# Performance work log

Measured on AMD Instinct MI355X. Metric: run time of the kernel, lower is better.

The kernel has to match this reference:

```python
import jax, jax.numpy as jnp
import numpy as np

# AdaptiveLogSoftmaxWithLoss config (input_dim=2048, n_classes=50257, div_value=4.0)
CUTOFFS = [1000, 10000, 50257]  # torch appends n_classes
N_CLUSTERS = 2                   # len(CUTOFFS) - 1
HEAD_SIZE = CUTOFFS[0] + N_CLUSTERS  # 1002
D = 2048
HSZ = [D // 4, D // 16]          # tail hidden sizes: [512, 128]
N_TOK = 4096


def setup_inputs() -> dict:
    key = jax.random.key(0)
    ks = jax.random.split(key, 7)
    w = 0.02  # weight scale so logits stay O(1)
    x = jax.random.normal(ks[0], (N_TOK, D), dtype=jnp.float32)
    W_head = jax.random.normal(ks[1], (HEAD_SIZE, D), dtype=jnp.float32) * w
    W1_0 = jax.random.normal(ks[2], (HSZ[0], D), dtype=jnp.float32) * w
    W2_0 = jax.random.normal(ks[3], (CUTOFFS[1] - CUTOFFS[0], HSZ[0]), dtype=jnp.float32) * w  # [9000, 512]
    W1_1 = jax.random.normal(ks[4], (HSZ[1], D), dtype=jnp.float32) * w
    W2_1 = jax.random.normal(ks[5], (CUTOFFS[2] - CUTOFFS[1], HSZ[1]), dtype=jnp.float32) * w  # [40257, 128]
    target = jax.random.randint(ks[6], (N_TOK,), 0, CUTOFFS[2], dtype=jnp.int32)
    return {"x": x, "target": target, "W_head": W_head,
            "W1_0": W1_0, "W2_0": W2_0, "W1_1": W1_1, "W2_1": W2_1}


def reference(x, target, W_head, W1_0, W2_0, W1_1, W2_1):
    # head: [N, 1002] = [1000 frequent classes | 2 cluster logits]
    head = x @ W_head.T
    head_lsm = jax.nn.log_softmax(head, axis=-1)

    t = target
    # log-prob of target if it lies in the head (clip keeps gather in-range; masked later)
    head_lp = jnp.take_along_axis(head_lsm, jnp.clip(t, 0, CUTOFFS[0] - 1)[:, None], axis=1)[:, 0]

    def tail_target_lp(W1, W2, low, high, cluster_idx):
        # two-stage projection: [N,D] @ [D,h] @ [h,osz]
        logits = (x @ W1.T) @ W2.T                     # [N, high-low]
        lsm = jax.nn.log_softmax(logits, axis=-1)
        idx = jnp.clip(t - low, 0, high - low - 1)
        g = jnp.take_along_axis(lsm, idx[:, None], axis=1)[:, 0]
        # combine with head's cluster log-prob
        return head_lsm[:, CUTOFFS[0] + cluster_idx] + g

    lp0 = tail_target_lp(W1_0, W2_0, CUTOFFS[0], CUTOFFS[1], 0)
    lp1 = tail_target_lp(W1_1, W2_1, CUTOFFS[1], CUTOFFS[2], 1)

    out = jnp.where(t < CUTOFFS[0], head_lp, jnp.where(t < CUTOFFS[1], lp0, lp1))
    loss = -jnp.mean(out)
    return out, loss
```

## Files before the change

kernel.cpp:

```cpp
#include <hip/hip_runtime.h>
#include <hip/hip_bf16.h>
#include <math.h>

#define NTOK 4096
#define DIM 2048
#define NHEAD 1002
#define NCAT 1664
#define C0LO 1000
#define C0HI 10000
#define OSZ0 9000
#define OSZ1 40257
#define H0S 512
#define H1S 128
#define JS0 32
#define JS1 16
#define HEADBLKS 8
#define NT0 141
#define NT1 315
#define PROJB 416
#define CVTB 352

typedef __attribute__((ext_vector_type(4))) short short4v;
typedef __attribute__((ext_vector_type(8))) short short8v;
typedef __attribute__((ext_vector_type(4))) float f32x4;
typedef __hip_bfloat16 bf16;

#define GLOBAL_AS __attribute__((address_space(1)))
#define LDS_AS __attribute__((address_space(3)))

#define RAW_BAR() __builtin_amdgcn_s_barrier()
#define SCHED_FENCE() __builtin_amdgcn_sched_barrier(0)
#define WAIT_VM(N) asm volatile("s_waitcnt vmcnt(" #N ")" ::: "memory")
#define WAIT_LGKM0() asm volatile("s_waitcnt lgkmcnt(0)" ::: "memory")

__device__ __forceinline__ int kperm(int c) {
  return (c & ~31) | (((c & 15) >> 2) << 3) | (((c >> 4) & 1) << 2) | (c & 3);
}

__device__ __forceinline__ void cvt8(const float* s1, const float* s2, bf16* dst) {
  union { short8v v; bf16 h[8]; } u;
  float4 a = *reinterpret_cast<const float4*>(s1);
  float4 b = *reinterpret_cast<const float4*>(s2);
  u.h[0] = __float2bfloat16(a.x); u.h[1] = __float2bfloat16(a.y);
  u.h[2] = __float2bfloat16(a.z); u.h[3] = __float2bfloat16(a.w);
  u.h[4] = __float2bfloat16(b.x); u.h[5] = __float2bfloat16(b.y);
  u.h[6] = __float2bfloat16(b.z); u.h[7] = __float2bfloat16(b.w);
  *reinterpret_cast<short8v*>(dst) = u.v;
}

__global__ __launch_bounds__(256) void cvt_xw(
    const float* __restrict__ x, const float* __restrict__ W_head,
    const float* __restrict__ W1_0, const float* __restrict__ W1_1,
    bf16* __restrict__ xb, bf16* __restrict__ Wcat) {
  const long NX = (long)NTOK * DIM / 8;
  const long NC = (long)NCAT * DIM / 8;
  long gid = (long)blockIdx.x * 256 + threadIdx.x;
  if (gid < NX) {
    long rel = gid * 8;
    long c1 = (rel & ~31L) + ((rel >> 3) & 3) * 4;
    cvt8(x + c1, x + c1 + 16, xb + rel);
  } else if (gid < NX + NC) {
    long rel = (gid - NX) * 8;
    int row = (int)(rel >> 11);
    long c1 = (rel & ~31L) + ((rel >> 3) & 3) * 4;
    int col = (int)(c1 & 2047);
    const float* srow = nullptr;
    if (row < NHEAD) srow = W_head + (long)row * DIM;
    else if (row < 1024) srow = nullptr;
    else if (row < 1536) srow = W1_0 + (long)(row - 1024) * DIM;
    else srow = W1_1 + (long)(row - 1536) * DIM;
    if (srow) {
      cvt8(srow + col, srow + col + 16, Wcat + rel);
    } else {
      union { short8v v; bf16 h[8]; } u;
#pragma unroll
      for (int e = 0; e < 8; ++e) u.h[e] = __float2bfloat16(0.f);
      *reinterpret_cast<short8v*>(Wcat + rel) = u.v;
    }
  }
}

__device__ __forceinline__ void stage_tile(const bf16* __restrict__ g, int row0,
                                           int maxrow, int ld, int k0,
                                           char* lds, int wave, int lane) {
#pragma unroll
  for (int c = 0; c < 4; ++c) {
    int rbase = wave * 32 + c * 8;
    int row = rbase + (lane >> 3);
    int grow = row0 + row;
    grow = grow < maxrow ? grow : maxrow;
    int slot = (lane & 7) ^ (row & 7);
    const bf16* src = g + (size_t)grow * ld + k0 + slot * 8;
    __builtin_amdgcn_global_load_lds((const GLOBAL_AS unsigned int*)src,
                                     (LDS_AS unsigned int*)(lds + rbase * 128),
                                     16, 0, 0);
  }
}

__device__ __forceinline__ void stage_tileB64(const bf16* __restrict__ g, int row0,
                                              int maxrow, int ld, int k0,
                                              char* lds, int wave, int lane) {
#pragma unroll
  for (int c = 0; c < 2; ++c) {
    int rbase = wave * 16 + c * 8;
    int row = rbase + (lane >> 3);
    int grow = row0 + row;
    grow = grow < maxrow ? grow : maxrow;
    int slot = (lane & 7) ^ (row & 7);
    const bf16* src = g + (size_t)grow * ld + k0 + slot * 8;
    __builtin_amdgcn_global_load_lds((const GLOBAL_AS unsigned int*)src,
                                     (LDS_AS unsigned int*)(lds + rbase * 128),
                                     16, 0, 0);
  }
}

__device__ __forceinline__ void stage_tile256(const bf16* __restrict__ g, int row0,
                                              int maxrow, int ld,
                                              char* lds, int wave, int lane) {
#pragma unroll
  for (int c = 0; c < 8; ++c) {
    int rbase = wave * 32 + c * 4;
    int row = rbase + (lane >> 4);
    int grow = row0 + row;
    grow = grow < maxrow ? grow : maxrow;
    int slot = (lane & 15) ^ (row & 7);
    const bf16* src = g + (size_t)grow * ld + slot * 8;
    __builtin_amdgcn_global_load_lds((const GLOBAL_AS unsigned int*)src,
                                     (LDS_AS unsigned int*)(lds + rbase * 256),
                                     16, 0, 0);
  }
}

__device__ __forceinline__ short8v read_frag(const char* lds, int row, int kk, int lane) {
  int slot = (kk * 4 + (lane >> 4)) ^ (row & 7);
  return *reinterpret_cast<const short8v*>(lds + row * 128 + slot * 16);
}
__device__ __forceinline__ short8v read_frag256(const char* lds, int row, int kk, int lane) {
  int slot = (kk * 4 + (lane >> 4)) ^ (row & 7);
  return *reinterpret_cast<const short8v*>(lds + row * 256 + slot * 16);
}

__device__ __forceinline__ void reduce_write_ps(float srun[4][4], float* reds,
                                                float* ps, int slice, int tok0,
                                                int lane, int wr, int wc) {
#pragma unroll
  for (int off = 1; off < 16; off <<= 1)
#pragma unroll
    for (int m = 0; m < 4; ++m)
#pragma unroll
      for (int r = 0; r < 4; ++r) srun[m][r] += __shfl_xor(srun[m][r], off);
  __syncthreads();
  if (wc == 0 && (lane & 15) == 0) {
#pragma unroll
    for (int m = 0; m < 4; ++m)
#pragma unroll
      for (int r = 0; r < 4; ++r)
        reds[wr * 64 + m * 16 + (lane >> 4) * 4 + r] = srun[m][r];
  }
  __syncthreads();
  if (wc == 1 && (lane & 15) == 0) {
#pragma unroll
    for (int m = 0; m < 4; ++m)
#pragma unroll
      for (int r = 0; r < 4; ++r) {
        int row = wr * 64 + m * 16 + (lane >> 4) * 4 + r;
        ps[(size_t)slice * NTOK + tok0 + row] = reds[row] + srun[m][r];
      }
  }
}

__global__ __launch_bounds__(256, 4) void tail0_lse(
    const bf16* __restrict__ Ab, const bf16* __restrict__ W2b,
    float* __restrict__ ps) {
  __shared__ __align__(16) char As[16384];
  __shared__ __align__(16) char Bs[8192];
  __shared__ float reds[128];
  int tid = threadIdx.x;
  int lane = tid & 63, wave = tid >> 6;
  int wr = wave >> 1, wc = wave & 1;
  int tok0 = blockIdx.x * 128;
  int ys = blockIdx.y;
  int t_lo = (NT0 * ys) / JS0, t_hi = (NT0 * (ys + 1)) / JS0;
  float srun[4][4] = {};
  for (int jt = t_lo; jt < t_hi; ++jt) {
    int j0 = jt * 64;
    f32x4 acc[4][2] = {};
    for (int k0 = 0; k0 < H0S; k0 += 64) {
      __syncthreads();
      stage_tile(Ab, tok0, NTOK - 1, H0S, k0, As, wave, lane);
      stage_tileB64(W2b, j0, OSZ0 - 1, H0S, k0, Bs, wave, lane);
      __syncthreads();
#pragma unroll
      for (int kk = 0; kk < 2; ++kk) {
        short8v af[4], bfr[2];
#pragma unroll
        for (int m = 0; m < 4; ++m)
          af[m] = read_frag(As, wr * 64 + m * 16 + (lane & 15), kk, lane);
#pragma unroll
        for (int n = 0; n < 2; ++n)
          bfr[n] = read_frag(Bs, wc * 32 + n * 16 + (lane & 15), kk, lane);
#pragma unroll
        for (int m = 0; m < 4; ++m)
#pragma unroll
          for (int n = 0; n < 2; ++n)
            acc[m][n] = __builtin_amdgcn_mfma_f32_16x16x32_bf16(af[m], bfr[n], acc[m][n], 0, 0, 0);
      }
    }
#pragma unroll
    for (int m = 0; m < 4; ++m)
#pragma unroll
      for (int n = 0; n < 2; ++n) {
        int col = j0 + wc * 32 + n * 16 + (lane & 15);
        if (col < OSZ0) {
#pragma unroll
          for (int r = 0; r < 4; ++r) srun[m][r] += __expf(acc[m][n][r]);
        }
      }
  }
  reduce_write_ps(srun, reds, ps, ys, tok0, lane, wr, wc);
}

__device__ void tail1_body(const bf16* __restrict__ Ab, const bf16* __restrict__ W2b,
                           float* __restrict__ ps, char* lds) {
  char* buf0 = lds;
  char* buf1 = lds + 32768;
  float* reds = (float*)(lds + 65536);
  int tid = threadIdx.x;
  int lane = tid & 63, wave = tid >> 6;
  int wr = wave >> 1, wc = wave & 1;
  int tok0 = blockIdx.x * 128;
  int ys = blockIdx.y;
  int t_lo = (NT1 * ys) / JS1, t_hi = (NT1 * (ys + 1)) / JS1;
  int nt = t_hi - t_lo;

  stage_tile256(Ab, tok0, NTOK - 1, H1S, buf1, wave, lane);
  WAIT_VM(0); SCHED_FENCE();
  RAW_BAR();
  short8v afr[4][4];
#pragma unroll
  for (int kk = 0; kk < 4; ++kk)
#pragma unroll
    for (int m = 0; m < 4; ++m)
      afr[kk][m] = read_frag256(buf1, wr * 64 + m * 16 + (lane & 15), kk, lane);
  stage_tile256(W2b, t_lo * 128, OSZ1 - 1, H1S, buf0, wave, lane);
  WAIT_LGKM0(); SCHED_FENCE();
  RAW_BAR();
  if (nt > 1) stage_tile256(W2b, (t_lo + 1) * 128, OSZ1 - 1, H1S, buf1, wave, lane);

  float srun[4][4] = {};
  for (int i = 0; i < nt; ++i) {
    char* cur = (i & 1) ? buf1 : buf0;
    if (i + 1 < nt) { WAIT_VM(8); } else { WAIT_VM(0); }
    SCHED_FENCE();
    RAW_BAR();
    int j0 = (t_lo + i) * 128;
    f32x4 acc[4][4] = {};
#pragma unroll
    for (int kk = 0; kk < 4; ++kk) {
      short8v bfr[4];
#pragma unroll
      for (int n = 0; n < 4; ++n)
        bfr[n] = read_frag256(cur, wc * 64 + n * 16 + (lane & 15), kk, lane);
#pragma unroll
      for (int m = 0; m < 4; ++m)
#pragma unroll
        for (int n = 0; n < 4; ++n)
          acc[m][n] = __builtin_amdgcn_mfma_f32_16x16x32_bf16(afr[kk][m], bfr[n], acc[m][n], 0, 0, 0);
    }
#pragma unroll
    for (int m = 0; m < 4; ++m)
#pragma unroll
      for (int n = 0; n < 4; ++n) {
        int col = j0 + wc * 64 + n * 16 + (lane & 15);
        if (col < OSZ1) {
#pragma unroll
          for (int r = 0; r < 4; ++r) srun[m][r] += __expf(acc[m][n][r]);
        }
      }
    SCHED_FENCE();
    RAW_BAR();
    if (i + 2 < nt) stage_tile256(W2b, (t_lo + i + 2) * 128, OSZ1 - 1, H1S, cur, wave, lane);
  }
  reduce_write_ps(srun, reds, ps, ys, tok0, lane, wr, wc);
}

__global__ __launch_bounds__(256, 2) void tail1_lse(
    const bf16* __restrict__ Ab, const bf16* __restrict__ W2b,
    float* __restrict__ ps) {
  __shared__ __align__(16) char lds[66048];
  tail1_body(Ab, W2b, ps, lds);
}

__global__ __launch_bounds__(256, 3) void proj_plus(
    const bf16* __restrict__ A, const bf16* __restrict__ B,
    const float* __restrict__ W2_0, const float* __restrict__ W2_1,
    bf16* __restrict__ W20b, bf16* __restrict__ W21b,
    float* __restrict__ head, float* __restrict__ h0, bf16* __restrict__ h0b,
    float* __restrict__ h1, bf16* __restrict__ h1b, float* __restrict__ ps_head) {
  __shared__ __align__(16) char As[16384];
  __shared__ __align__(16) char Bs[16384];
  __shared__ float reds[128];
  if (blockIdx.x >= PROJB) {
    const long N20 = (long)OSZ0 * H0S / 8;
    const long N21 = (long)OSZ1 * H1S / 8;
    long idx = (long)(blockIdx.x - PROJB) * 256 + threadIdx.x;
    const long stride = (long)CVTB * 256;
    for (; idx < N20 + N21; idx += stride) {
      long rel; const float* srcb; bf16* dstb;
      if (idx < N20) { rel = idx * 8;          srcb = W2_0; dstb = W20b; }
      else           { rel = (idx - N20) * 8;  srcb = W2_1; dstb = W21b; }
      long c1 = (rel & ~31L) + ((rel >> 3) & 3) * 4;
      cvt8(srcb + c1, srcb + c1 + 16, dstb + rel);
    }
    return;
  }
  int tid = threadIdx.x;
  int lane = tid & 63, wave = tid >> 6;
  int wr = wave >> 1, wc = wave & 1;
  int wgid = blockIdx.x;
  int cx = wgid & 7, w = wgid >> 3;
  int col_b = w >> 2;
  int row_b = cx * 4 + (w & 3);
  int row0 = row_b * 128, col0 = col_b * 128;
  f32x4 acc[4][4] = {};
  for (int k0 = 0; k0 < DIM; k0 += 64) {
    __syncthreads();
    stage_tile(A, row0, NTOK - 1, DIM, k0, As, wave, lane);
    stage_tile(B, col0, NCAT - 1, DIM, k0, Bs, wave, lane);
    __syncthreads();
#pragma unroll
    for (int kk = 0; kk < 2; ++kk) {
      short8v af[4], bfr[4];
#pragma unroll
      for (int m = 0; m < 4; ++m)
        af[m] = read_frag(As, wr * 64 + m * 16 + (lane & 15), kk, lane);
#pragma unroll
      for (int n = 0; n < 4; ++n)
        bfr[n] = read_frag(Bs, wc * 64 + n * 16 + (lane & 15), kk, lane);
#pragma unroll
      for (int m = 0; m < 4; ++m)
#pragma unroll
        for (int n = 0; n < 4; ++n)
          acc[m][n] = __builtin_amdgcn_mfma_f32_16x16x32_bf16(af[m], bfr[n], acc[m][n], 0, 0, 0);
    }
  }
  float srun[4][4] = {};
#pragma unroll
  for (int m = 0; m < 4; ++m) {
    int row = row0 + wr * 64 + m * 16 + (lane >> 4) * 4;
#pragma unroll
    for (int n = 0; n < 4; ++n) {
      int col = col0 + wc * 64 + n * 16 + (lane & 15);
#pragma unroll
      for (int r = 0; r < 4; ++r) {
        float v = acc[m][n][r];
        if (col < NHEAD) {
          head[(size_t)(row + r) * NHEAD + col] = v;
          srun[m][r] += __expf(v);
        } else if (col >= 1024 && col < 1536) {
          int c = col - 1024;
          h0[(size_t)(row + r) * H0S + c] = v;
          h0b[(size_t)(row + r) * H0S + kperm(c)] = __float2bfloat16(v);
        } else if (col >= 1536) {
          int c = col - 1536;
          h1[(size_t)(row + r) * H1S + c] = v;
          h1b[(size_t)(row + r) * H1S + kperm(c)] = __float2bfloat16(v);
        }
      }
    }
  }
  if (col_b < HEADBLKS) {
    reduce_write_ps(srun, reds, ps_head, col_b, row0, lane, wr, wc);
  }
}

__global__ __launch_bounds__(256) void finalize2(
    const int* __restrict__ target, const float* __restrict__ head,
    const float* __restrict__ ps_head,
    const float* __restrict__ h0, const float* __restrict__ h1,
    const float* __restrict__ W2_0, const float* __restrict__ W2_1,
    const float* __restrict__ ps0, const float* __restrict__ ps1,
    float* __restrict__ out) {
  int warp = threadIdx.x >> 6, lane = threadIdx.x & 63;
  int i = blockIdx.x * 4 + warp;
  if (i >= NTOK) return;
  int t = target[i];
  float sh = 0.f;
#pragma unroll
  for (int s = 0; s < HEADBLKS; ++s) sh += ps_head[(size_t)s * NTOK + i];
  float lse_head = logf(sh);
  float res;
  if (t < C0LO) {
    res = head[(size_t)i * NHEAD + t] - lse_head;
  } else {
    int c = (t < C0HI) ? 0 : 1;
    int H = c ? H1S : H0S;
    int low = c ? C0HI : C0LO;
    const float* hv = (c ? h1 : h0) + (size_t)i * H;
    const float* wv = (c ? W2_1 : W2_0) + (size_t)(t - low) * H;
    float p = 0.f;
    for (int k = lane * 4; k < H; k += 256) {
      float4 a = *reinterpret_cast<const float4*>(hv + k);
      float4 b = *reinterpret_cast<const float4*>(wv + k);
      p += a.x * b.x + a.y * b.y + a.z * b.z + a.w * b.w;
    }
#pragma unroll
    for (int off = 32; off > 0; off >>= 1) p += __shfl_xor(p, off);
    const float* ps = c ? ps1 : ps0;
    int js = c ? JS1 : JS0;
    float S = 0.f;
    for (int s = 0; s < js; ++s) S += ps[(size_t)s * NTOK + i];
    float cl = head[(size_t)i * NHEAD + C0LO + c];
    res = (cl - lse_head) + (p - logf(S));
  }
  if (lane == 0) out[i] = res;
}

__global__ __launch_bounds__(256) void loss_kernel(float* __restrict__ out) {
  __shared__ float red[256];
  int tid = threadIdx.x;
  float s = 0.f;
  for (int j = tid; j < NTOK; j += 256) s += out[j];
  red[tid] = s; __syncthreads();
  for (int off = 128; off > 0; off >>= 1) {
    if (tid < off) red[tid] += red[tid + off];
    __syncthreads();
  }
  if (tid == 0) out[NTOK] = -red[0] / (float)NTOK;
}

extern "C" void kernel_launch(void* const* d_in, const int* in_sizes, int n_in,
                              void* d_out, int out_size, void* d_ws, size_t ws_size,
                              hipStream_t stream) {
  (void)in_sizes; (void)n_in; (void)out_size; (void)ws_size;
  const float* x = (const float*)d_in[0];
  const int* target = (const int*)d_in[1];
  const float* W_head = (const float*)d_in[2];
  const float* W1_0 = (const float*)d_in[3];
  const float* W2_0 = (const float*)d_in[4];
  const float* W1_1 = (const float*)d_in[5];
  const float* W2_1 = (const float*)d_in[6];
  float* out = (float*)d_out;

  char* w = (char*)d_ws;
  size_t off = 0;
  auto alloc = [&](size_t bytes) -> void* {
    void* p = w + off;
    off = (off + bytes + 255) & ~(size_t)255;
    return p;
  };
  bf16* xb   = (bf16*)alloc((size_t)NTOK * DIM * 2);
  bf16* Wcat = (bf16*)alloc((size_t)NCAT * DIM * 2);
  bf16* W20b = (bf16*)alloc((size_t)OSZ0 * H0S * 2);
  bf16* W21b = (bf16*)alloc((size_t)OSZ1 * H1S * 2);
  float* head = (float*)alloc((size_t)NTOK * NHEAD * 4);
  float* h0   = (float*)alloc((size_t)NTOK * H0S * 4);
  bf16*  h0b  = (bf16*)alloc((size_t)NTOK * H0S * 2);
  float* h1   = (float*)alloc((size_t)NTOK * H1S * 4);
  bf16*  h1b  = (bf16*)alloc((size_t)NTOK * H1S * 2);
  float* ps_head = (float*)alloc((size_t)HEADBLKS * NTOK * 4);
  float* ps0 = (float*)alloc((size_t)JS0 * NTOK * 4);
  float* ps1 = (float*)alloc((size_t)JS1 * NTOK * 4);

  dim3 blk(256);
  const long NXW = (long)NTOK * DIM / 8 + (long)NCAT * DIM / 8;
  cvt_xw<<<dim3((unsigned)((NXW + 255) / 256)), blk, 0, stream>>>(
      x, W_head, W1_0, W1_1, xb, Wcat);

  proj_plus<<<dim3(PROJB + CVTB), blk, 0, stream>>>(
      xb, Wcat, W2_0, W2_1, W20b, W21b, head, h0, h0b, h1, h1b, ps_head);

  tail0_lse<<<dim3(NTOK / 128, JS0), blk, 0, stream>>>(h0b, W20b, ps0);
  tail1_lse<<<dim3(NTOK / 128, JS1), blk, 0, stream>>>(h1b, W21b, ps1);

  finalize2<<<dim3(NTOK / 4), blk, 0, stream>>>(target, head, ps_head, h0, h1,
                                                W2_0, W2_1, ps0, ps1, out);
  loss_kernel<<<1, blk, 0, stream>>>(out);
}
```

Before: 174.9 us.

## Widen tail1 blocks to 8 waves covering 256 tokens per W2 tile

```diff
diff --git a/kernel.cpp b/kernel.cpp
--- a/kernel.cpp
+++ b/kernel.cpp
@@ -13,7 +13,7 @@
 #define H0S 512
 #define H1S 128
 #define JS0 32
-#define JS1 16
+#define JS1 32
 #define HEADBLKS 8
 #define NT0 141
 #define NT1 315
@@ -114,12 +114,29 @@
   }
 }
 
-__device__ __forceinline__ void stage_tile256(const bf16* __restrict__ g, int row0,
+__device__ __forceinline__ void stage_A256_w8(const bf16* __restrict__ g, int row0,
                                               int maxrow, int ld,
                                               char* lds, int wave, int lane) {
 #pragma unroll
   for (int c = 0; c < 8; ++c) {
     int rbase = wave * 32 + c * 4;
+    int row = rbase + (lane >> 4);
+    int grow = row0 + row;
+    grow = grow < maxrow ? grow : maxrow;
+    int slot = (lane & 15) ^ (row & 7);
+    const bf16* src = g + (size_t)grow * ld + slot * 8;
+    __builtin_amdgcn_global_load_lds((const GLOBAL_AS unsigned int*)src,
+                                     (LDS_AS unsigned int*)(lds + rbase * 256),
+                                     16, 0, 0);
+  }
+}
+
+__device__ __forceinline__ void stage_B128_w8(const bf16* __restrict__ g, int row0,
+                                              int maxrow, int ld,
+                                              char* lds, int wave, int lane) {
+#pragma unroll
+  for (int c = 0; c < 4; ++c) {
+    int rbase = wave * 16 + c * 4;
     int row = rbase + (lane >> 4);
     int grow = row0 + row;
     grow = grow < maxrow ? grow : maxrow;
@@ -228,12 +245,12 @@
   int tid = threadIdx.x;
   int lane = tid & 63, wave = tid >> 6;
   int wr = wave >> 1, wc = wave & 1;
-  int tok0 = blockIdx.x * 128;
+  int tok0 = blockIdx.x * 256;
   int ys = blockIdx.y;
   int t_lo = (NT1 * ys) / JS1, t_hi = (NT1 * (ys + 1)) / JS1;
   int nt = t_hi - t_lo;
 
-  stage_tile256(Ab, tok0, NTOK - 1, H1S, buf1, wave, lane);
+  stage_A256_w8(Ab, tok0, NTOK - 1, H1S, lds, wave, lane);
   WAIT_VM(0); SCHED_FENCE();
   RAW_BAR();
   short8v afr[4][4];
@@ -241,16 +258,16 @@
   for (int kk = 0; kk < 4; ++kk)
 #pragma unroll
     for (int m = 0; m < 4; ++m)
-      afr[kk][m] = read_frag256(buf1, wr * 64 + m * 16 + (lane & 15), kk, lane);
-  stage_tile256(W2b, t_lo * 128, OSZ1 - 1, H1S, buf0, wave, lane);
+      afr[kk][m] = read_frag256(lds, wr * 64 + m * 16 + (lane & 15), kk, lane);
   WAIT_LGKM0(); SCHED_FENCE();
   RAW_BAR();
-  if (nt > 1) stage_tile256(W2b, (t_lo + 1) * 128, OSZ1 - 1, H1S, buf1, wave, lane);
+  stage_B128_w8(W2b, t_lo * 128, OSZ1 - 1, H1S, buf0, wave, lane);
+  if (nt > 1) stage_B128_w8(W2b, (t_lo + 1) * 128, OSZ1 - 1, H1S, buf1, wave, lane);
 
   float srun[4][4] = {};
   for (int i = 0; i < nt; ++i) {
     char* cur = (i & 1) ? buf1 : buf0;
-    if (i + 1 < nt) { WAIT_VM(8); } else { WAIT_VM(0); }
+    if (i + 1 < nt) { WAIT_VM(4); } else { WAIT_VM(0); }
     SCHED_FENCE();
     RAW_BAR();
     int j0 = (t_lo + i) * 128;
@@ -279,15 +296,15 @@
       }
     SCHED_FENCE();
     RAW_BAR();
-    if (i + 2 < nt) stage_tile256(W2b, (t_lo + i + 2) * 128, OSZ1 - 1, H1S, cur, wave, lane);
+    if (i + 2 < nt) stage_B128_w8(W2b, (t_lo + i + 2) * 128, OSZ1 - 1, H1S, cur, wave, lane);
   }
   reduce_write_ps(srun, reds, ps, ys, tok0, lane, wr, wc);
 }
 
-__global__ __launch_bounds__(256, 2) void tail1_lse(
+__global__ __launch_bounds__(512, 4) void tail1_lse(
     const bf16* __restrict__ Ab, const bf16* __restrict__ W2b,
     float* __restrict__ ps) {
-  __shared__ __align__(16) char lds[66048];
+  __shared__ __align__(16) char lds[66560];
   tail1_body(Ab, W2b, ps, lds);
 }
 
@@ -471,7 +488,7 @@
       xb, Wcat, W2_0, W2_1, W20b, W21b, head, h0, h0b, h1, h1b, ps_head);
 
   tail0_lse<<<dim3(NTOK / 128, JS0), blk, 0, stream>>>(h0b, W20b, ps0);
-  tail1_lse<<<dim3(NTOK / 128, JS1), blk, 0, stream>>>(h1b, W21b, ps1);
+  tail1_lse<<<dim3(NTOK / 256, JS1), dim3(512), 0, stream>>>(h1b, W21b, ps1);
 
   finalize2<<<dim3(NTOK / 4), blk, 0, stream>>>(target, head, ps_head, h0, h1,
                                                 W2_0, W2_1, ps0, ps1, out);
```

Result: slower. 243.3 us (+39.1%).
